# Kernel tuning notes

Hardware: AMD Instinct MI355X
Metric: run time of the kernel (lower is better)

## Reference

```python
import jax, jax.numpy as jnp
import numpy as np
import math

NZ, NX, NY = 4, 2048, 2048
DX = DY = 4000.0


def dstI1D(x):
    # type-I discrete sine transform along last axis (ortho norm) via irfft
    n = x.shape[-1]
    pad = [(0, 0)] * (x.ndim - 1) + [(1, 1)]
    return jnp.fft.irfft(-1j * jnp.pad(x, pad), axis=-1, norm='ortho')[..., 1:n + 1]


def dstI2D(x):
    # DST-I over the last two axes
    x = dstI1D(x)
    x = jnp.swapaxes(dstI1D(jnp.swapaxes(x, -1, -2)), -1, -2)
    return x


def inverse_elliptic_dstI(f, helmholtz_dst):
    # DST-I is its own inverse with ortho norm: solve in spectral space
    return dstI2D(dstI2D(f) / helmholtz_dst)


def center_avg_2D(x):
    return 0.25 * (x[..., 1:, 1:] + x[..., 1:, :-1] + x[..., :-1, 1:] + x[..., :-1, :-1])


def _build_solver_constants(beta):
    # create_helmholtz_dst
    x, y = jnp.meshgrid(jnp.arange(1, NY), jnp.arange(1, NX), indexing='ij')
    L_mat = (2 * (jnp.cos(math.pi / NX * x) - 1) / DX ** 2
             + 2 * (jnp.cos(math.pi / NY * y) - 1) / DY ** 2)
    H_mat = (L_mat[None] - beta[:, None, None]).astype(jnp.float32)  # [Nz, Nx-1, Ny-1]
    # compute_homogeneous_solution
    ones_int = jnp.ones((NZ, NX - 1, NY - 1), jnp.float32)
    sol = inverse_elliptic_dstI(ones_int, H_mat)
    sol = jnp.pad(sol, ((0, 0), (1, 1), (1, 1)))  # [Nz, Nx+1, Ny+1]
    homsol = jnp.ones((NZ, NX + 1, NY + 1), jnp.float32) + sol * beta[:, None, None]
    homsol_mean = jnp.mean(center_avg_2D(homsol), axis=(-2, -1))  # mask = all ones
    return H_mat, homsol.astype(jnp.float32), homsol_mean.astype(jnp.float32)


def setup_inputs() -> dict:
    key = jax.random.key(0)
    k1, k2 = jax.random.split(key)
    q = jax.random.normal(k1, (NZ, NX - 1, NY - 1), jnp.float32)
    # mode<->layer change of basis (Mode2LayerTransformer): Cm2l = inv(Cl2m)
    A = jax.random.normal(k2, (NZ, NZ), jnp.float32) * 0.3 + jnp.eye(NZ, dtype=jnp.float32)
    Cl2m = A
    Cm2l = jnp.linalg.inv(A).astype(jnp.float32)
    # lambda_sq eigenvalues (1/deformation-radius^2), first barotropic mode ~ 0
    beta = jnp.array([0.0, 1.0e-9, 4.0e-9, 1.0e-8], jnp.float32)
    H_mat, homsol, homsol_mean = _build_solver_constants(beta)
    return {'q': q, 'Cl2m': Cl2m, 'Cm2l': Cm2l,
            'helmholtz_mat': H_mat, 'homsol': homsol, 'homsol_mean': homsol_mean}


def reference(q, Cl2m, Cm2l, helmholtz_mat, homsol, homsol_mean):
    # layer -> mode
    src_modes = jnp.einsum('ml,lxy->mxy', Cl2m, q)
    # spectral elliptic solve per mode (Nz batched over leading axis)
    psi_modes = inverse_elliptic_dstI(src_modes, helmholtz_mat)
    psi_modes = jnp.pad(psi_modes, ((0, 0), (1, 1), (1, 1)))  # [Nz, Nx+1, Ny+1]
    # homogeneous-solution correction to enforce zero mean
    psi_modes_mean = jnp.mean(center_avg_2D(psi_modes), axis=(-2, -1))
    alpha = -psi_modes_mean / homsol_mean
    psi_modes = psi_modes + alpha[:, None, None] * homsol
    # mode -> layer
    psi = jnp.einsum('lm,mxy->lxy', Cm2l, psi_modes)
    return psi
```

## Files before the change

### kernel.cpp

```cpp
#include <hip/hip_runtime.h>


typedef __attribute__((ext_vector_type(8))) short bf16x8;
typedef __attribute__((ext_vector_type(4))) float f32x4;
typedef __attribute__((ext_vector_type(8))) unsigned short ushort8;

#define LDS_SPACE __attribute__((address_space(3)))
#define GLB_SPACE __attribute__((address_space(1)))

__device__ __forceinline__ void gld_lds16(const unsigned short* g, unsigned short* l) {
  __builtin_amdgcn_global_load_lds((const GLB_SPACE void*)g, (LDS_SPACE void*)l, 16, 0, 0);
}

__device__ __forceinline__ bf16x8 ds_read128(const void* p) {
  bf16x8 r;
  const LDS_SPACE char* lp = (const LDS_SPACE char*)p;
  asm volatile("ds_read_b128 %0, %1" : "=v"(r) : "v"(lp));
  return r;
}

__device__ __forceinline__ float sinrev(float rev) {
  float r;
  asm("v_sin_f32 %0, %1" : "=v"(r) : "v"(rev));
  return r;
}

__device__ __forceinline__ unsigned short f2b(float f) {
  union { float f; unsigned u; } v; v.f = f;
  unsigned r = (v.u + 0x7fffu + ((v.u >> 16) & 1u)) >> 16;
  return (unsigned short)r;
}
__device__ __forceinline__ float b2f(unsigned short u) {
  union { unsigned u; float f; } v; v.u = ((unsigned)u) << 16;
  return v.f;
}

#define LGKM(N) asm volatile("s_waitcnt lgkmcnt(" #N ")" ::: "memory")
#define VMC(N)  asm volatile("s_waitcnt vmcnt(" #N ")" ::: "memory")
#define BAR()   __builtin_amdgcn_s_barrier()
#define SB0()   __builtin_amdgcn_sched_barrier(0)
#define PRIO1() __builtin_amdgcn_s_setprio(1)
#define PRIO0() __builtin_amdgcn_s_setprio(0)

__global__ __launch_bounds__(256)
void tables_kernel(unsigned short* __restrict__ T) {
  const int idx = blockIdx.x * 256 + threadIdx.x;
  const int tbl = idx >> 20, n = (idx >> 10) & 1023, k = idx & 1023;
  int a;
  if (tbl < 2) a = k;
  else a = (k < 512) ? 2 * k : (k < 1023 ? 2 * (k - 512) + 1 : 1023);
  const int cp1 = (tbl & 1) ? 2 * n + 2 : 2 * n + 1;
  const int ph = ((a + 1) * cp1) & 4095;
  const float v = 0.03125f * sinf(3.14159265358979323846f * (float)ph * (1.0f / 2048.0f));
  T[idx] = f2b(v);
}

__global__ __launch_bounds__(256)
void mix_fold(const float* __restrict__ q, const float* __restrict__ Cl2m,
              unsigned short* __restrict__ AE, unsigned short* __restrict__ AO) {
  const int idx = blockIdx.x * 256 + threadIdx.x;
  const int x = idx >> 10, u = idx & 1023;
  float c[16];
#pragma unroll
  for (int i = 0; i < 16; ++i) c[i] = Cl2m[i];
  float fe[4] = {0.f, 0.f, 0.f, 0.f}, fo[4] = {0.f, 0.f, 0.f, 0.f};
  if (x < 2047) {
#pragma unroll
    for (int l = 0; l < 4; ++l) {
      const size_t base = ((size_t)l * 2047 + x) * 2047;
      const float qa = q[base + u];
      const float qb = (u < 1023) ? q[base + 2046 - u] : 0.f;
      const float E = (u == 1023) ? qa : qa + qb;
      const float O = (u == 1023) ? 0.f : qa - qb;
#pragma unroll
      for (int m = 0; m < 4; ++m) { fe[m] += c[m * 4 + l] * E; fo[m] += c[m * 4 + l] * O; }
    }
  }
#pragma unroll
  for (int m = 0; m < 4; ++m) {
    AE[((size_t)m * 2048 + x) * 1024 + u] = f2b(fe[m]);
    AO[((size_t)m * 2048 + x) * 1024 + u] = f2b(fo[m]);
  }
}

template <int MAP>
__global__ __launch_bounds__(256)
void tfold(const unsigned short* __restrict__ in, unsigned short* __restrict__ outE,
           unsigned short* __restrict__ outO) {
  __shared__ unsigned short t1[64][72];
  __shared__ unsigned short t2[64][72];
  const size_t ib = (size_t)blockIdx.z * (2048u * 2048u);
  const size_t ob = (size_t)blockIdx.z * (2048u * 1024u);
  const int c0 = blockIdx.x * 64, u0 = blockIdx.y * 64;
  const int t = threadIdx.x;
  const int rr = t >> 3, cc = (t & 7) * 8;
#pragma unroll
  for (int ch = 0; ch < 2; ++ch) {
    const int r = ch * 32 + rr, u = u0 + r;
    const int r1 = (MAP == 0) ? u : (u < 512 ? u : 1024 + (u - 512));
    const int r2 = (MAP == 0) ? 2046 - u : (u < 512 ? 1023 - u : 2046 - (u - 512));
    ushort8 v1 = *(const ushort8*)&in[ib + (size_t)r1 * 2048 + c0 + cc];
    ushort8 v2 = *(const ushort8*)&in[ib + (size_t)r2 * 2048 + c0 + cc];
#pragma unroll
    for (int j = 0; j < 8; ++j) { t1[r][cc + j] = v1[j]; t2[r][cc + j] = v2[j]; }
  }
  __syncthreads();
#pragma unroll
  for (int ch = 0; ch < 2; ++ch) {
    const int r = ch * 32 + rr;
    ushort8 vE, vO;
#pragma unroll
    for (int j = 0; j < 8; ++j) {
      const int uu = u0 + cc + j;
      const float a = b2f(t1[cc + j][r]);
      const float b = b2f(t2[cc + j][r]);
      vE[j] = f2b((uu == 1023) ? a : a + b);
      vO[j] = f2b((uu == 1023) ? 0.f : a - b);
    }
    const size_t o = ob + (size_t)(c0 + r) * 1024 + u0 + cc;
    *(ushort8*)&outE[o] = vE;
    *(ushort8*)&outO[o] = vO;
  }
}

__global__ __launch_bounds__(256)
void fold_cols(const unsigned short* __restrict__ R, unsigned short* __restrict__ AE,
               unsigned short* __restrict__ AO) {
  const int idx = blockIdx.x * 256 + threadIdx.x;
  const int row = idx >> 10, u = idx & 1023;
  const int c1 = (u < 512) ? u : (u < 1023 ? 512 + u : 1535);
  const int c2 = (u < 512) ? 1023 - u : (u < 1023 ? 2558 - u : 1535);
  const float a = b2f(R[(size_t)row * 2048 + c1]);
  const float b = b2f(R[(size_t)row * 2048 + c2]);
  AE[(size_t)row * 1024 + u] = f2b((u == 1023) ? a : a + b);
  AO[(size_t)row * 1024 + u] = f2b((u == 1023) ? 0.f : a - b);
}

#define MFMA_BF16 __builtin_amdgcn_mfma_f32_16x16x32_bf16

template <int EPI>
__global__ __launch_bounds__(256, 3)
void gemm_eo(const unsigned short* __restrict__ A, const unsigned short* __restrict__ T,
             unsigned short* __restrict__ Cb, const float* __restrict__ H,
             float* __restrict__ sums) {
  __shared__ __align__(16) char lds[32768];
  const int bid = blockIdx.x;
  const int swz = (bid & 7) * 128 + (bid >> 3);
  const int h = swz & 1;
  const int bn = (swz >> 1) & 7, bm = swz >> 4;
  const int tid = threadIdx.x;
  const int lane = tid & 63, wave = tid >> 6;
  const int wr = wave >> 1, wc = wave & 1;
  const int lr = lane & 15, kg = lane >> 4;
  const int x2 = (lr ^ (lr >> 2)) & 3;

  const unsigned short* gA = A + (size_t)h * 8388608u + (size_t)bm * 128 * 1024;
  const unsigned short* gB = T + (size_t)h * 1048576u + (size_t)bn * 128 * 1024;

  auto stage = [&](int kt, int c) {
    char* lcA = lds + c * 8192;
    char* lcB = lds + 16384 + c * 8192;
    const int ko = kt * 32;
#pragma unroll
    for (int i = 0; i < 2; ++i) {
      const int ps = tid + i * 256;
      const int row = ps >> 2;
      const int k16 = (ps & 3) ^ ((row ^ (row >> 2)) & 3);
      gld_lds16(gA + (size_t)row * 1024 + ko + k16 * 8,
                (unsigned short*)(lcA + ps * 16));
    }
#pragma unroll
    for (int i = 0; i < 2; ++i) {
      const int ps = tid + i * 256;
      const int row = ps >> 2;
      const int k16 = (ps & 3) ^ ((row ^ (row >> 2)) & 3);
      gld_lds16(gB + (size_t)row * 1024 + ko + k16 * 8,
                (unsigned short*)(lcB + ps * 16));
    }
  };

  f32x4 acc[4][4];
#pragma unroll
  for (int m = 0; m < 4; ++m)
#pragma unroll
    for (int n = 0; n < 4; ++n) acc[m][n] = (f32x4){0.f, 0.f, 0.f, 0.f};

  stage(0, 0);
  stage(1, 1);

  const int arow = wr * 64 + lr;
  const int brow = wc * 64 + lr;
  const int rdoff = ((kg ^ x2) << 4);

  for (int t = 0; t < 32; ++t) {
    const char* la = lds + (t & 1) * 8192;
    const char* lb = lds + 16384 + (t & 1) * 8192;
    if (t < 31) { VMC(4); } else { VMC(0); }
    BAR();

    bf16x8 av[4], bv[4];
#pragma unroll
    for (int i = 0; i < 4; ++i)
      av[i] = ds_read128(la + (arow + i * 16) * 64 + rdoff);
#pragma unroll
    for (int j = 0; j < 4; ++j)
      bv[j] = ds_read128(lb + (brow + j * 16) * 64 + rdoff);
    LGKM(0); SB0();
    BAR();

    if (t < 30) stage(t + 2, t & 1);

    PRIO1();
#pragma unroll
    for (int mi = 0; mi < 4; ++mi)
#pragma unroll
      for (int ni = 0; ni < 4; ++ni)
        acc[mi][ni] = MFMA_BF16(av[mi], bv[ni], acc[mi][ni], 0, 0, 0);
    PRIO0();
  }

  LGKM(0); VMC(0);
  __syncthreads();

  float beta = 0.f, tA[4];
  bool iok[4] = {true, true, true, true};
  if (EPI == 1) {
    const float s1 = sinrev(1.0f / 8192.0f);
    beta = -5.0e-7f * s1 * s1 - H[(size_t)(bm >> 4) * 4190209u];
#pragma unroll
    for (int n = 0; n < 4; ++n) {
      const int ia = 2 * (bn * 128 + wc * 64 + n * 16 + lr) + h;
      iok[n] = ia < 2047;
      const float s = sinrev((float)(ia + 1) * (1.0f / 8192.0f));
      tA[n] = -2.5e-7f * s * s;
    }
  }

  float ssum = 0.f;
#pragma unroll
  for (int m = 0; m < 4; ++m) {
#pragma unroll
    for (int j = 0; j < 4; ++j) {
      const int row_l = wr * 64 + m * 16 + kg * 4 + j;
      float tB = 0.f;
      bool jok = true;
      if (EPI == 1) {
        const int jint = (bm * 128 + row_l) & 2047;
        const int j_true = 2 * (jint & 1023) + (jint >> 10);
        jok = j_true < 2047;
        const float s = sinrev((float)(j_true + 1) * (1.0f / 8192.0f));
        tB = -2.5e-7f * s * s;
      }
#pragma unroll
      for (int n = 0; n < 4; ++n) {
        const int col_l = wc * 64 + n * 16 + lr;
        float v = acc[m][n][j];
        if (EPI == 1) {
          const float Hv = tA[n] + tB - beta;
          float r = __builtin_amdgcn_rcpf(Hv);
          r = r * (2.0f - Hv * r);
          v = (iok[n] && jok) ? v * r : 0.f;
        }
        if (EPI == 2) ssum += v;
        const int byte = row_l * 256 + ((((col_l >> 3) ^ (row_l & 7)) << 4)) + (col_l & 7) * 2;
        *(unsigned short*)&lds[byte] = f2b(v);
      }
    }
  }
  __syncthreads();

  unsigned short* gC = Cb + (size_t)(bm * 128) * 2048 + h * 1024 + bn * 128;
#pragma unroll
  for (int p = 0; p < 8; ++p) {
    const int c = p * 256 + tid;
    const int r = c >> 4, c16 = c & 15;
    const bf16x8 vv = *(const bf16x8*)&lds[r * 256 + ((c16 ^ (r & 7)) << 4)];
    *(bf16x8*)&gC[(size_t)r * 2048 + c16 * 8] = vv;
  }

  if (EPI == 2) {
#pragma unroll
    for (int off = 32; off > 0; off >>= 1) ssum += __shfl_xor(ssum, off);
    if (lane == 0) atomicAdd(&sums[bm >> 4], ssum);
  }
}

__global__ __launch_bounds__(256)
void final_kernel(const unsigned short* __restrict__ V, const float* __restrict__ homsol,
                  const float* __restrict__ hm, const float* __restrict__ Cm2l,
                  const float* __restrict__ sums, float* __restrict__ out) {
  const int p = blockIdx.x * 256 + threadIdx.x;
  if (p >= 2049 * 2049) return;
  const int x = p / 2049, y = p - x * 2049;
  const bool interior = (x >= 1) && (x <= 2047) && (y >= 1) && (y <= 2047);
  int row = 0, col = 0;
  if (interior) {
    const int xt = x - 1, yt = y - 1;
    row = (xt & 1) ? 1024 + (xt >> 1) : (xt >> 1);
    col = (yt & 1) ? 1024 + (yt >> 1) : (yt >> 1);
  }
  float pm[4];
#pragma unroll
  for (int m = 0; m < 4; ++m) {
    float inner = 0.f;
    if (interior) inner = b2f(V[((size_t)m * 2048 + row) * 2048 + col]);
    const float alpha = -(sums[m] * (1.0f / 4194304.0f)) / hm[m];
    pm[m] = inner + alpha * homsol[(size_t)m * 4198401u + p];
  }
#pragma unroll
  for (int l = 0; l < 4; ++l) {
    out[(size_t)l * 4198401u + p] =
        Cm2l[l * 4 + 0] * pm[0] + Cm2l[l * 4 + 1] * pm[1] +
        Cm2l[l * 4 + 2] * pm[2] + Cm2l[l * 4 + 3] * pm[3];
  }
}

extern "C" void kernel_launch(void* const* d_in, const int* in_sizes, int n_in,
                              void* d_out, int out_size, void* d_ws, size_t ws_size,
                              hipStream_t stream) {
  const float* q     = (const float*)d_in[0];
  const float* Cl2m  = (const float*)d_in[1];
  const float* Cm2l  = (const float*)d_in[2];
  const float* H     = (const float*)d_in[3];
  const float* hom   = (const float*)d_in[4];
  const float* hmean = (const float*)d_in[5];
  float* out = (float*)d_out;

  char* ws = (char*)d_ws;
  unsigned short* Tb = (unsigned short*)ws;
  unsigned short* Aslot = (unsigned short*)(ws + 8388608u);
  unsigned short* Bslot = (unsigned short*)(ws + 41943040u);
  float* sums        = (float*)(ws + 75497472u);
  unsigned short* AO = Aslot + 8388608u;

  tables_kernel<<<16384, 256, 0, stream>>>(Tb);
  mix_fold<<<8192, 256, 0, stream>>>(q, Cl2m, Aslot, AO);
  hipMemsetAsync(sums, 0, 16, stream);

  const dim3 tg(32, 16, 4);
  gemm_eo<0><<<1024, 256, 0, stream>>>(Aslot, Tb, Bslot, nullptr, nullptr);
  tfold<0><<<tg, 256, 0, stream>>>(Bslot, Aslot, AO);
  gemm_eo<1><<<1024, 256, 0, stream>>>(Aslot, Tb, Bslot, H, nullptr);
  fold_cols<<<32768, 256, 0, stream>>>(Bslot, Aslot, AO);
  gemm_eo<0><<<1024, 256, 0, stream>>>(Aslot, Tb + 2097152u, Bslot, nullptr, nullptr);
  tfold<1><<<tg, 256, 0, stream>>>(Bslot, Aslot, AO);
  gemm_eo<2><<<1024, 256, 0, stream>>>(Aslot, Tb + 2097152u, Bslot, nullptr, sums);

  final_kernel<<<16401, 256, 0, stream>>>(Bslot, hom, hmean, Cm2l, sums, out);
}
```

Baseline: 316.8 us.

## Widen GEMM tile to 128x256 with 8 waves and simplify the pipeline

The four DST GEMMs now run 512-thread blocks that compute 128x256 output tiles instead of 128x128. The LDS layout is reorganised around a new XOR swizzle, and the hand-written ds_read/waitcnt/setprio scheduling is replaced by plain LDS loads and __syncthreads. Each B tile is reused across more rows, so fewer blocks are launched and less global traffic is spent per output. In exchange there are only 512 blocks and the double-buffered load/compute overlap is weaker, because the stage for the next iteration is only issued after a full barrier. The sine table generator also switches from sinf to the hardware v_sin instruction.

```diff
diff --git a/kernel.cpp b/kernel.cpp
--- a/kernel.cpp
+++ b/kernel.cpp
@@ -10,13 +10,6 @@
 
 __device__ __forceinline__ void gld_lds16(const unsigned short* g, unsigned short* l) {
   __builtin_amdgcn_global_load_lds((const GLB_SPACE void*)g, (LDS_SPACE void*)l, 16, 0, 0);
-}
-
-__device__ __forceinline__ bf16x8 ds_read128(const void* p) {
-  bf16x8 r;
-  const LDS_SPACE char* lp = (const LDS_SPACE char*)p;
-  asm volatile("ds_read_b128 %0, %1" : "=v"(r) : "v"(lp));
-  return r;
 }
 
 __device__ __forceinline__ float sinrev(float rev) {
@@ -34,13 +27,6 @@
   union { unsigned u; float f; } v; v.u = ((unsigned)u) << 16;
   return v.f;
 }
-
-#define LGKM(N) asm volatile("s_waitcnt lgkmcnt(" #N ")" ::: "memory")
-#define VMC(N)  asm volatile("s_waitcnt vmcnt(" #N ")" ::: "memory")
-#define BAR()   __builtin_amdgcn_s_barrier()
-#define SB0()   __builtin_amdgcn_sched_barrier(0)
-#define PRIO1() __builtin_amdgcn_s_setprio(1)
-#define PRIO0() __builtin_amdgcn_s_setprio(0)
 
 __global__ __launch_bounds__(256)
 void tables_kernel(unsigned short* __restrict__ T) {
@@ -51,7 +37,7 @@
   else a = (k < 512) ? 2 * k : (k < 1023 ? 2 * (k - 512) + 1 : 1023);
   const int cp1 = (tbl & 1) ? 2 * n + 2 : 2 * n + 1;
   const int ph = ((a + 1) * cp1) & 4095;
-  const float v = 0.03125f * sinf(3.14159265358979323846f * (float)ph * (1.0f / 2048.0f));
+  const float v = 0.03125f * sinrev((float)ph * (1.0f / 4096.0f));
   T[idx] = f2b(v);
 }
 
@@ -139,42 +125,39 @@
 #define MFMA_BF16 __builtin_amdgcn_mfma_f32_16x16x32_bf16
 
 template <int EPI>
-__global__ __launch_bounds__(256, 3)
+__global__ __launch_bounds__(512, 2)
 void gemm_eo(const unsigned short* __restrict__ A, const unsigned short* __restrict__ T,
              unsigned short* __restrict__ Cb, const float* __restrict__ H,
              float* __restrict__ sums) {
-  __shared__ __align__(16) char lds[32768];
+  __shared__ __align__(16) char lds[65536];
   const int bid = blockIdx.x;
-  const int swz = (bid & 7) * 128 + (bid >> 3);
+  const int swz = (bid & 7) * 64 + (bid >> 3);
   const int h = swz & 1;
-  const int bn = (swz >> 1) & 7, bm = swz >> 4;
+  const int bn = (swz >> 1) & 3, bm = swz >> 3;
   const int tid = threadIdx.x;
   const int lane = tid & 63, wave = tid >> 6;
-  const int wr = wave >> 1, wc = wave & 1;
+  const int wr = wave >> 2, wc = wave & 3;
   const int lr = lane & 15, kg = lane >> 4;
-  const int x2 = (lr ^ (lr >> 2)) & 3;
 
   const unsigned short* gA = A + (size_t)h * 8388608u + (size_t)bm * 128 * 1024;
-  const unsigned short* gB = T + (size_t)h * 1048576u + (size_t)bn * 128 * 1024;
+  const unsigned short* gB = T + (size_t)h * 1048576u + (size_t)bn * 256 * 1024;
 
   auto stage = [&](int kt, int c) {
-    char* lcA = lds + c * 8192;
-    char* lcB = lds + 16384 + c * 8192;
-    const int ko = kt * 32;
+    char* lcA = lds + c * 24576;
+    char* lcB = lcA + 8192;
+    {
+      const int ps = tid;
+      const int pg = ps >> 3, p = (ps & 7) ^ (pg & 7);
+      const int row = 2 * pg + (p >> 2), k16 = p & 3;
+      gld_lds16(gA + (size_t)row * 1024 + kt * 32 + k16 * 8,
+                (unsigned short*)(lcA + ps * 16));
+    }
 #pragma unroll
     for (int i = 0; i < 2; ++i) {
-      const int ps = tid + i * 256;
-      const int row = ps >> 2;
-      const int k16 = (ps & 3) ^ ((row ^ (row >> 2)) & 3);
-      gld_lds16(gA + (size_t)row * 1024 + ko + k16 * 8,
-                (unsigned short*)(lcA + ps * 16));
-    }
-#pragma unroll
-    for (int i = 0; i < 2; ++i) {
-      const int ps = tid + i * 256;
-      const int row = ps >> 2;
-      const int k16 = (ps & 3) ^ ((row ^ (row >> 2)) & 3);
-      gld_lds16(gB + (size_t)row * 1024 + ko + k16 * 8,
+      const int ps = tid + i * 512;
+      const int pg = ps >> 3, p = (ps & 7) ^ (pg & 7);
+      const int row = 2 * pg + (p >> 2), k16 = p & 3;
+      gld_lds16(gB + (size_t)row * 1024 + kt * 32 + k16 * 8,
                 (unsigned short*)(lcB + ps * 16));
     }
   };
@@ -187,40 +170,35 @@
 
   stage(0, 0);
   stage(1, 1);
-
-  const int arow = wr * 64 + lr;
-  const int brow = wc * 64 + lr;
-  const int rdoff = ((kg ^ x2) << 4);
+  __syncthreads();
+
+  const LDS_SPACE char* lbase = (const LDS_SPACE char*)lds;
+
+  auto rdoff = [&](int row) {
+    return (row >> 1) * 128 + (((((row & 1) << 2) | kg) ^ ((row >> 1) & 7)) << 4);
+  };
 
   for (int t = 0; t < 32; ++t) {
-    const char* la = lds + (t & 1) * 8192;
-    const char* lb = lds + 16384 + (t & 1) * 8192;
-    if (t < 31) { VMC(4); } else { VMC(0); }
-    BAR();
+    const LDS_SPACE char* la = lbase + (t & 1) * 24576;
+    const LDS_SPACE char* lb = la + 8192;
 
     bf16x8 av[4], bv[4];
 #pragma unroll
-    for (int i = 0; i < 4; ++i)
-      av[i] = ds_read128(la + (arow + i * 16) * 64 + rdoff);
-#pragma unroll
-    for (int j = 0; j < 4; ++j)
-      bv[j] = ds_read128(lb + (brow + j * 16) * 64 + rdoff);
-    LGKM(0); SB0();
-    BAR();
-
+    for (int m = 0; m < 4; ++m)
+      av[m] = *(const LDS_SPACE bf16x8*)(la + rdoff(wr * 64 + m * 16 + lr));
+#pragma unroll
+    for (int n = 0; n < 4; ++n)
+      bv[n] = *(const LDS_SPACE bf16x8*)(lb + rdoff(wc * 64 + n * 16 + lr));
+
+#pragma unroll
+    for (int m = 0; m < 4; ++m)
+#pragma unroll
+      for (int n = 0; n < 4; ++n)
+        acc[m][n] = MFMA_BF16(av[m], bv[n], acc[m][n], 0, 0, 0);
+
+    __syncthreads();
     if (t < 30) stage(t + 2, t & 1);
-
-    PRIO1();
-#pragma unroll
-    for (int mi = 0; mi < 4; ++mi)
-#pragma unroll
-      for (int ni = 0; ni < 4; ++ni)
-        acc[mi][ni] = MFMA_BF16(av[mi], bv[ni], acc[mi][ni], 0, 0, 0);
-    PRIO0();
-  }
-
-  LGKM(0); VMC(0);
-  __syncthreads();
+  }
 
   float beta = 0.f, tA[4];
   bool iok[4] = {true, true, true, true};
@@ -229,7 +207,7 @@
     beta = -5.0e-7f * s1 * s1 - H[(size_t)(bm >> 4) * 4190209u];
 #pragma unroll
     for (int n = 0; n < 4; ++n) {
-      const int ia = 2 * (bn * 128 + wc * 64 + n * 16 + lr) + h;
+      const int ia = 2 * (bn * 256 + wc * 64 + n * 16 + lr) + h;
       iok[n] = ia < 2047;
       const float s = sinrev((float)(ia + 1) * (1.0f / 8192.0f));
       tA[n] = -2.5e-7f * s * s;
@@ -262,19 +240,19 @@
           v = (iok[n] && jok) ? v * r : 0.f;
         }
         if (EPI == 2) ssum += v;
-        const int byte = row_l * 256 + ((((col_l >> 3) ^ (row_l & 7)) << 4)) + (col_l & 7) * 2;
+        const int byte = row_l * 512 + ((((col_l >> 3) ^ (row_l & 7)) << 4)) + (col_l & 7) * 2;
         *(unsigned short*)&lds[byte] = f2b(v);
       }
     }
   }
   __syncthreads();
 
-  unsigned short* gC = Cb + (size_t)(bm * 128) * 2048 + h * 1024 + bn * 128;
+  unsigned short* gC = Cb + (size_t)(bm * 128) * 2048 + h * 1024 + bn * 256;
 #pragma unroll
   for (int p = 0; p < 8; ++p) {
-    const int c = p * 256 + tid;
-    const int r = c >> 4, c16 = c & 15;
-    const bf16x8 vv = *(const bf16x8*)&lds[r * 256 + ((c16 ^ (r & 7)) << 4)];
+    const int c = p * 512 + tid;
+    const int r = c >> 5, c16 = c & 31;
+    const bf16x8 vv = *(const bf16x8*)&lds[r * 512 + ((c16 ^ (r & 7)) << 4)];
     *(bf16x8*)&gC[(size_t)r * 2048 + c16 * 8] = vv;
   }
 
@@ -338,13 +316,13 @@
   hipMemsetAsync(sums, 0, 16, stream);
 
   const dim3 tg(32, 16, 4);
-  gemm_eo<0><<<1024, 256, 0, stream>>>(Aslot, Tb, Bslot, nullptr, nullptr);
+  gemm_eo<0><<<512, 512, 0, stream>>>(Aslot, Tb, Bslot, nullptr, nullptr);
   tfold<0><<<tg, 256, 0, stream>>>(Bslot, Aslot, AO);
-  gemm_eo<1><<<1024, 256, 0, stream>>>(Aslot, Tb, Bslot, H, nullptr);
+  gemm_eo<1><<<512, 512, 0, stream>>>(Aslot, Tb, Bslot, H, nullptr);
   fold_cols<<<32768, 256, 0, stream>>>(Bslot, Aslot, AO);
-  gemm_eo<0><<<1024, 256, 0, stream>>>(Aslot, Tb + 2097152u, Bslot, nullptr, nullptr);
+  gemm_eo<0><<<512, 512, 0, stream>>>(Aslot, Tb + 2097152u, Bslot, nullptr, nullptr);
   tfold<1><<<tg, 256, 0, stream>>>(Bslot, Aslot, AO);
-  gemm_eo<2><<<1024, 256, 0, stream>>>(Aslot, Tb + 2097152u, Bslot, nullptr, sums);
+  gemm_eo<2><<<512, 512, 0, stream>>>(Aslot, Tb + 2097152u, Bslot, nullptr, sums);
 
   final_kernel<<<16401, 256, 0, stream>>>(Bslot, hom, hmean, Cm2l, sums, out);
 }
```

After: 343.5 us. +8.4%, slower.
